# Optimization experiments

Measured on AMD Instinct MI355X. Metric: run time of the kernel, lower is better.

Reference implementation:

```python
import jax, jax.numpy as jnp
import numpy as np
import math

D_MODEL = 512
NUM_HEADS = 8
D_K = D_MODEL // NUM_HEADS
B, S = 4, 2048


def setup_inputs() -> dict:
    key = jax.random.key(0)
    ks = jax.random.split(key, 8)
    scale = 1.0 / math.sqrt(D_MODEL)
    return {
        "q": jax.random.normal(ks[0], (B, S, D_MODEL), jnp.float32),
        "k": jax.random.normal(ks[1], (B, S, D_MODEL), jnp.float32),
        "v": jax.random.normal(ks[2], (B, S, D_MODEL), jnp.float32),
        "mask": jax.random.randint(ks[3], (B, 1, S, S), 0, 2) > 0,
        "w_q": jax.random.normal(ks[4], (D_MODEL, D_MODEL), jnp.float32) * scale,
        "w_k": jax.random.normal(ks[5], (D_MODEL, D_MODEL), jnp.float32) * scale,
        "w_v": jax.random.normal(ks[6], (D_MODEL, D_MODEL), jnp.float32) * scale,
        "w_o": jax.random.normal(ks[7], (D_MODEL, D_MODEL), jnp.float32) * scale,
    }


def reference(q, k, v, mask, w_q, w_k, w_v, w_o):
    # Linear(d_model,d_model,bias=False): y = x @ W^T
    def split_heads(x):  # [B,S,D] -> [B,H,S,Dk]
        return x.reshape(B, S, NUM_HEADS, D_K).transpose(0, 2, 1, 3)

    queries = split_heads(q @ w_q.T)
    keys = split_heads(k @ w_k.T)
    values = split_heads(v @ w_v.T)

    scores = jnp.einsum("bhqd,bhkd->bhqk", queries, keys) / math.sqrt(D_K)
    scores = jnp.where(mask, jnp.float32(-1e9), scores)
    attention_weights = jax.nn.softmax(scores, axis=-1)  # [B,H,S,S]

    attn = jnp.einsum("bhqk,bhkd->bhqd", attention_weights, values)
    attn = attn.transpose(0, 2, 1, 3).reshape(B, S, D_MODEL)
    out = attn @ w_o.T
    return out, attention_weights
```

## Files before the change

### kernel.cpp

```cpp
#include <hip/hip_runtime.h>
#include <hip/hip_bf16.h>
#include <cstdint>

constexpr int B_ = 4;
constexpr int S_ = 2048;
constexpr int D_ = 512;
constexpr int H_ = 8;
constexpr int DK_ = 64;
constexpr int M_ = B_ * S_;

typedef __attribute__((ext_vector_type(8))) short bf16x8;
typedef __attribute__((ext_vector_type(4))) short bf16x4;
typedef __attribute__((ext_vector_type(4))) float f32x4;

__device__ __forceinline__ unsigned short f2bf(float x) {
    unsigned u = __float_as_uint(x);
    return (unsigned short)((u + 0x7fffu + ((u >> 16) & 1u)) >> 16);
}
__device__ __forceinline__ float bf2f(unsigned short h) {
    return __uint_as_float(((unsigned)h) << 16);
}

#define MFMA32(a, b, c) __builtin_amdgcn_mfma_f32_16x16x32_bf16(a, b, c, 0, 0, 0)

__global__ __launch_bounds__(256) void cvt_rm(const float* __restrict__ X,
                                              short* __restrict__ Xh,
                                              short* __restrict__ Xl) {
    size_t idx = ((size_t)blockIdx.x * 256 + threadIdx.x) * 8;
    float4 v0 = *reinterpret_cast<const float4*>(X + idx);
    float4 v1 = *reinterpret_cast<const float4*>(X + idx + 4);
    float f[8] = {v0.x, v0.y, v0.z, v0.w, v1.x, v1.y, v1.z, v1.w};
    short hh[8], ll[8];
#pragma unroll
    for (int e = 0; e < 8; ++e) {
        unsigned short hb = f2bf(f[e]);
        hh[e] = (short)hb;
        ll[e] = (short)f2bf(f[e] - bf2f(hb));
    }
    *(bf16x4*)(Xh + idx)     = (bf16x4){hh[0], hh[1], hh[2], hh[3]};
    *(bf16x4*)(Xh + idx + 4) = (bf16x4){hh[4], hh[5], hh[6], hh[7]};
    *(bf16x4*)(Xl + idx)     = (bf16x4){ll[0], ll[1], ll[2], ll[3]};
    *(bf16x4*)(Xl + idx + 4) = (bf16x4){ll[4], ll[5], ll[6], ll[7]};
}

__device__ __forceinline__ void stage_bf(const short* __restrict__ srcH,
                                         const short* __restrict__ srcL,
                                         short* Hh, short* Hl, int tid, int rows) {
#pragma unroll
    for (int p = 0; p < rows / 32; ++p) {
        int idx = tid + p * 256;
        int r = idx >> 3;
        int cc = idx & 7;
        int off = r * 64 + ((cc ^ (r & 7)) << 3);
        *(bf16x8*)(Hh + off) = *(const bf16x8*)(srcH + (size_t)r * 512 + cc * 8);
        *(bf16x8*)(Hl + off) = *(const bf16x8*)(srcL + (size_t)r * 512 + cc * 8);
    }
}

template <int EPI>
__global__ __launch_bounds__(256) void gemm_bf(const short* __restrict__ Ah_g,
                                               const short* __restrict__ Al_g,
                                               const short* __restrict__ Wh_g,
                                               const short* __restrict__ Wl_g,
                                               float* __restrict__ C,
                                               short* __restrict__ Ch,
                                               short* __restrict__ Cl) {
    __shared__ __align__(16) short Ah[8192];
    __shared__ __align__(16) short Al[8192];
    __shared__ __align__(16) short Wh[4096];
    __shared__ __align__(16) short Wl[4096];

    const int tid = threadIdx.x;
    const int wave = tid >> 6;
    const int lane = tid & 63;
    const int lg = lane >> 4;
    const int lr = lane & 15;
    const int bm = blockIdx.x * 128;
    const int bn = blockIdx.y * 64;

    f32x4 acc[2][4];
#pragma unroll
    for (int s = 0; s < 2; ++s)
#pragma unroll
        for (int n = 0; n < 4; ++n) acc[s][n] = (f32x4){0.f, 0.f, 0.f, 0.f};

    for (int k0 = 0; k0 < 512; k0 += 64) {
        stage_bf(Ah_g + (size_t)bm * 512 + k0, Al_g + (size_t)bm * 512 + k0, Ah, Al, tid, 128);
        stage_bf(Wh_g + (size_t)bn * 512 + k0, Wl_g + (size_t)bn * 512 + k0, Wh, Wl, tid, 64);
        __syncthreads();

#pragma unroll
        for (int ks = 0; ks < 2; ++ks) {
            bf16x8 ah[2], al[2];
#pragma unroll
            for (int sub = 0; sub < 2; ++sub) {
                int r = wave * 32 + sub * 16 + lr;
                int off = r * 64 + (((ks * 4 + lg) ^ (r & 7)) << 3);
                ah[sub] = *(const bf16x8*)(Ah + off);
                al[sub] = *(const bf16x8*)(Al + off);
            }
#pragma unroll
            for (int nsub = 0; nsub < 4; ++nsub) {
                int r = nsub * 16 + lr;
                int off = r * 64 + (((ks * 4 + lg) ^ (r & 7)) << 3);
                bf16x8 wh = *(const bf16x8*)(Wh + off);
                bf16x8 wl = *(const bf16x8*)(Wl + off);
#pragma unroll
                for (int sub = 0; sub < 2; ++sub) {
                    acc[sub][nsub] = MFMA32(ah[sub], wh, acc[sub][nsub]);
                    acc[sub][nsub] = MFMA32(ah[sub], wl, acc[sub][nsub]);
                    acc[sub][nsub] = MFMA32(al[sub], wh, acc[sub][nsub]);
                }
            }
        }
        __syncthreads();
    }

#pragma unroll
    for (int sub = 0; sub < 2; ++sub)
#pragma unroll
        for (int nsub = 0; nsub < 4; ++nsub)
#pragma unroll
            for (int rr = 0; rr < 4; ++rr) {
                int row = bm + wave * 32 + sub * 16 + lg * 4 + rr;
                int col = bn + nsub * 16 + lr;
                float a = acc[sub][nsub][rr];
                if (EPI == 0) {
                    C[(size_t)row * 512 + col] = a;
                } else {
                    unsigned short hb = f2bf(a);
                    size_t off = (((size_t)(row >> 11) * 8 + (col >> 6)) * 2048 +
                                  (row & 2047)) * 64 + (col & 63);
                    Ch[off] = (short)hb;
                    Cl[off] = (short)f2bf(a - bf2f(hb));
                }
            }
}

__global__ __launch_bounds__(256) void vt_kernel(const float* __restrict__ V,
                                                 short* __restrict__ Vt) {
    __shared__ short tile[64][72];
    const int bh = blockIdx.y;
    const int b = bh >> 3, h = bh & 7;
    const int j0 = blockIdx.x * 64;
    const int tid = threadIdx.x;
    {
        int jj = tid >> 2;
        int c = (tid & 3) * 16;
        const float* src = V + ((size_t)(b * 2048 + j0 + jj)) * 512 + h * 64 + c;
#pragma unroll
        for (int q = 0; q < 4; ++q) {
            float4 v = *reinterpret_cast<const float4*>(src + q * 4);
            tile[jj][c + q * 4 + 0] = (short)f2bf(v.x);
            tile[jj][c + q * 4 + 1] = (short)f2bf(v.y);
            tile[jj][c + q * 4 + 2] = (short)f2bf(v.z);
            tile[jj][c + q * 4 + 3] = (short)f2bf(v.w);
        }
    }
    __syncthreads();
    {
        int dk = tid >> 2;
        int jq = (tid & 3) * 16;
        short* dst = Vt + ((size_t)(bh * 64 + dk)) * 2048 + j0 + jq;
#pragma unroll
        for (int q = 0; q < 4; ++q) {
            bf16x4 o = {tile[jq + q * 4 + 0][dk], tile[jq + q * 4 + 1][dk],
                        tile[jq + q * 4 + 2][dk], tile[jq + q * 4 + 3][dk]};
            *(bf16x4*)(dst + q * 4) = o;
        }
    }
}

__global__ __launch_bounds__(256) void mask_pack(const int* __restrict__ mask,
                                                 unsigned long long* __restrict__ pk) {
    const int row = blockIdx.x;
    const int tid = threadIdx.x;
    const int* mrow = mask + (size_t)row * 2048;
#pragma unroll
    for (int p = 0; p < 8; ++p) {
        int j = p * 256 + tid;
        unsigned long long bal = __ballot(mrow[j] != 0);
        if ((tid & 63) == 0) pk[(size_t)row * 32 + p * 4 + (tid >> 6)] = bal;
    }
}

__global__ __launch_bounds__(256, 3) void fused_attn(
    const short* __restrict__ Qh_g, const short* __restrict__ Ql_g,
    const short* __restrict__ Kh_g, const short* __restrict__ Kl_g,
    const short* __restrict__ Vt_g, const unsigned long long* __restrict__ pk,
    float* __restrict__ P, short* __restrict__ Aho, short* __restrict__ Alo) {
    __shared__ __align__(16) short Kbuf[2][2][4096];
    __shared__ __align__(16) short Wt[4096];

    const int tid = threadIdx.x;
    const int wave = tid >> 6;
    const int lane = tid & 63;
    const int lg = lane >> 4;
    const int lr = lane & 15;

    const int wgid = blockIdx.y * 32 + blockIdx.x;
    const int xcd = wgid & 7;
    const int slot = wgid >> 3;
    const int bh = xcd * 4 + (slot & 3);
    const int i0 = (slot >> 2) * 64;
    const int b = bh >> 3;

    bf16x8 qh[2], ql[2];
    {
        const size_t qbase = ((size_t)bh * 2048 + i0 + wave * 16 + lr) * 64;
#pragma unroll
        for (int ks = 0; ks < 2; ++ks) {
            qh[ks] = *(const bf16x8*)(Qh_g + qbase + (ks * 4 + lg) * 8);
            ql[ks] = *(const bf16x8*)(Ql_g + qbase + (ks * 4 + lg) * 8);
        }
    }

    const int o0 = tid * 16;
    const int o1 = 4096 + tid * 16;
    const int s0 = o0 ^ (((o0 >> 7) & 7) << 4);
    const int s1 = o1 ^ (((o1 >> 7) & 7) << 4);

    bf16x8 Rh0, Rh1, Rl0, Rl1;
#define LOADKH(t)                                                           \
    {                                                                       \
        const short* bKh = Kh_g + ((size_t)bh * 2048 + (t) * 64) * 64;      \
        Rh0 = *(const bf16x8*)(bKh + (o0 >> 1));                            \
        Rh1 = *(const bf16x8*)(bKh + (o1 >> 1));                            \
    }
#define WRITEKH(cur)                                                        \
    {                                                                       \
        *(bf16x8*)(&Kbuf[cur][0][0] + (s0 >> 1)) = Rh0;                     \
        *(bf16x8*)(&Kbuf[cur][0][0] + (s1 >> 1)) = Rh1;                     \
    }
#define LOADK(t)                                                            \
    {                                                                       \
        const short* bKh = Kh_g + ((size_t)bh * 2048 + (t) * 64) * 64;      \
        const short* bKl = Kl_g + ((size_t)bh * 2048 + (t) * 64) * 64;      \
        Rh0 = *(const bf16x8*)(bKh + (o0 >> 1));                            \
        Rh1 = *(const bf16x8*)(bKh + (o1 >> 1));                            \
        Rl0 = *(const bf16x8*)(bKl + (o0 >> 1));                            \
        Rl1 = *(const bf16x8*)(bKl + (o1 >> 1));                            \
    }
#define WRITEK(cur)                                                         \
    {                                                                       \
        *(bf16x8*)(&Kbuf[cur][0][0] + (s0 >> 1)) = Rh0;                     \
        *(bf16x8*)(&Kbuf[cur][0][0] + (s1 >> 1)) = Rh1;                     \
        *(bf16x8*)(&Kbuf[cur][1][0] + (s0 >> 1)) = Rl0;                     \
        *(bf16x8*)(&Kbuf[cur][1][0] + (s1 >> 1)) = Rl1;                     \
    }

    const size_t pkrow = (size_t)b * 2048 + i0 + wave * 16 + lg * 4;

    float l_[4] = {0.f, 0.f, 0.f, 0.f};

    LOADKH(0);
    for (int t = 0; t < 32; ++t) {
        const int cur = t & 1;
        WRITEKH(cur);
        if (t < 31) LOADKH(t + 1);
        unsigned long long pkv[4];
#pragma unroll
        for (int rr = 0; rr < 4; ++rr) pkv[rr] = pk[(pkrow + rr) * 32 + t];
        __syncthreads();

        const short* KH = &Kbuf[cur][0][0];
#pragma unroll
        for (int jt = 0; jt < 4; ++jt) {
            f32x4 s = (f32x4){0.f, 0.f, 0.f, 0.f};
            int r = jt * 16 + lr;
#pragma unroll
            for (int ks = 0; ks < 2; ++ks) {
                int off = (r * 128 + (ks * 4 + lg) * 16) ^ ((r & 7) << 4);
                bf16x8 kh = *(const bf16x8*)(KH + (off >> 1));
                s = MFMA32(qh[ks], kh, s);
            }
#pragma unroll
            for (int rr = 0; rr < 4; ++rr) {
                bool mk = (pkv[rr] >> (jt * 16 + lr)) & 1ull;
                l_[rr] += mk ? 0.f : __expf(s[rr] * 0.125f);
            }
        }
    }

#pragma unroll
    for (int rr = 0; rr < 4; ++rr) {
        float l = l_[rr];
#pragma unroll
        for (int d = 1; d < 16; d <<= 1) l += __shfl_xor(l, d);
        l_[rr] = l;
    }

    float invl[4];
#pragma unroll
    for (int rr = 0; rr < 4; ++rr) invl[rr] = 1.0f / fmaxf(l_[rr], 1e-37f);

    f32x4 Oa[4];
#pragma unroll
    for (int dt = 0; dt < 4; ++dt) Oa[dt] = (f32x4){0.f, 0.f, 0.f, 0.f};

    LOADK(0);
    for (int t = 0; t < 32; ++t) {
        const int cur = t & 1;
        WRITEK(cur);
        if (t < 31) LOADK(t + 1);
        unsigned long long pkv[4];
#pragma unroll
        for (int rr = 0; rr < 4; ++rr) pkv[rr] = pk[(pkrow + rr) * 32 + t];
        bf16x8 vf[4][2];
#pragma unroll
        for (int dt = 0; dt < 4; ++dt)
#pragma unroll
            for (int ks2 = 0; ks2 < 2; ++ks2)
                vf[dt][ks2] = *(const bf16x8*)(Vt_g +
                    ((size_t)(bh * 64 + dt * 16 + lr)) * 2048 + t * 64 + (ks2 * 4 + lg) * 8);
        __syncthreads();

        const short* KH = &Kbuf[cur][0][0];
        const short* KL = &Kbuf[cur][1][0];
#pragma unroll
        for (int jt = 0; jt < 4; ++jt) {
            f32x4 s = (f32x4){0.f, 0.f, 0.f, 0.f};
            int r = jt * 16 + lr;
#pragma unroll
            for (int ks = 0; ks < 2; ++ks) {
                int off = (r * 128 + (ks * 4 + lg) * 16) ^ ((r & 7) << 4);
                bf16x8 kh = *(const bf16x8*)(KH + (off >> 1));
                bf16x8 kl = *(const bf16x8*)(KL + (off >> 1));
                s = MFMA32(qh[ks], kh, s);
                s = MFMA32(qh[ks], kl, s);
                s = MFMA32(ql[ks], kh, s);
            }
#pragma unroll
            for (int rr = 0; rr < 4; ++rr) {
                bool mk = (pkv[rr] >> (jt * 16 + lr)) & 1ull;
                float w = mk ? 0.f : __expf(s[rr] * 0.125f) * invl[rr];
                int rw = wave * 16 + lg * 4 + rr;
                int wo = rw * 64 + (((jt * 2 + (lr >> 3)) ^ (rw & 7)) << 3) + (lr & 7);
                Wt[wo] = (short)f2bf(w);
            }
        }

        {
            int rp = wave * 16 + (lane >> 2);
            int c2 = (lane & 3) * 2;
            int po0 = rp * 64 + (((c2 + 0) ^ (rp & 7)) << 3);
            int po1 = rp * 64 + (((c2 + 1) ^ (rp & 7)) << 3);
            bf16x8 wa = *(const bf16x8*)(Wt + po0);
            bf16x8 wb = *(const bf16x8*)(Wt + po1);
            float* Prow = P + ((size_t)bh * 2048 + i0 + rp) * 2048 + t * 64 + (lane & 3) * 16;
#pragma unroll
            for (int q = 0; q < 2; ++q) {
                f32x4 oA = {bf2f((unsigned short)wa[q * 4 + 0]), bf2f((unsigned short)wa[q * 4 + 1]),
                            bf2f((unsigned short)wa[q * 4 + 2]), bf2f((unsigned short)wa[q * 4 + 3])};
                f32x4 oB = {bf2f((unsigned short)wb[q * 4 + 0]), bf2f((unsigned short)wb[q * 4 + 1]),
                            bf2f((unsigned short)wb[q * 4 + 2]), bf2f((unsigned short)wb[q * 4 + 3])};
                *(f32x4*)(Prow + q * 4) = oA;
                *(f32x4*)(Prow + 8 + q * 4) = oB;
            }
        }

        bf16x8 aw[2];
#pragma unroll
        for (int ks2 = 0; ks2 < 2; ++ks2) {
            int ra = wave * 16 + lr;
            int ao = ra * 64 + (((ks2 * 4 + lg) ^ (ra & 7)) << 3);
            aw[ks2] = *(const bf16x8*)(Wt + ao);
        }
#pragma unroll
        for (int dt = 0; dt < 4; ++dt)
#pragma unroll
            for (int ks2 = 0; ks2 < 2; ++ks2)
                Oa[dt] = MFMA32(aw[ks2], vf[dt][ks2], Oa[dt]);
    }

    {
        const int h = bh & 7;
#pragma unroll
        for (int dt = 0; dt < 4; ++dt)
#pragma unroll
            for (int rr = 0; rr < 4; ++rr) {
                int gi = i0 + wave * 16 + lg * 4 + rr;
                size_t off = ((size_t)(b * 2048 + gi)) * 512 + h * 64 + dt * 16 + lr;
                float a = Oa[dt][rr];
                unsigned short hb = f2bf(a);
                Aho[off] = (short)hb;
                Alo[off] = (short)f2bf(a - bf2f(hb));
            }
    }
#undef LOADKH
#undef WRITEKH
#undef LOADK
#undef WRITEK
}

extern "C" void kernel_launch(void* const* d_in, const int* in_sizes, int n_in,
                              void* d_out, int out_size, void* d_ws, size_t ws_size,
                              hipStream_t stream) {
    const float* q   = (const float*)d_in[0];
    const float* k   = (const float*)d_in[1];
    const float* v   = (const float*)d_in[2];
    const int*   msk = (const int*)d_in[3];
    const float* w_q = (const float*)d_in[4];
    const float* w_k = (const float*)d_in[5];
    const float* w_v = (const float*)d_in[6];
    const float* w_o = (const float*)d_in[7];

    float* out = (float*)d_out;
    float* P   = out + (size_t)B_ * S_ * D_;

    short* qh = (short*)d_ws;
    short* ql = qh + (size_t)4194304;
    short* kh = ql + (size_t)4194304;
    short* kl = kh + (size_t)4194304;
    short* vh = kl + (size_t)4194304;
    short* vl = vh + (size_t)4194304;
    short* Qh = vl + (size_t)4194304;
    short* Ql = Qh + (size_t)4194304;
    short* Kh = Ql + (size_t)4194304;
    short* Kl = Kh + (size_t)4194304;
    float* Vf = (float*)(Kl + (size_t)4194304);
    short* Vt = (short*)(Vf + (size_t)M_ * D_);
    unsigned long long* pk = (unsigned long long*)(Vt + (size_t)4194304);
    short* wqh = (short*)(pk + (size_t)262144);
    short* wql = wqh + (size_t)262144;
    short* wkh = wql + (size_t)262144;
    short* wkl = wkh + (size_t)262144;
    short* wvh = wkl + (size_t)262144;
    short* wvl = wvh + (size_t)262144;
    short* woh = wvl + (size_t)262144;
    short* wol = woh + (size_t)262144;

    dim3 blk(256);
    dim3 gproj(M_ / 128, D_ / 64);

    hipLaunchKernelGGL(cvt_rm, dim3(2048), blk, 0, stream, q, qh, ql);
    hipLaunchKernelGGL(cvt_rm, dim3(2048), blk, 0, stream, k, kh, kl);
    hipLaunchKernelGGL(cvt_rm, dim3(2048), blk, 0, stream, v, vh, vl);
    hipLaunchKernelGGL(cvt_rm, dim3(128), blk, 0, stream, w_q, wqh, wql);
    hipLaunchKernelGGL(cvt_rm, dim3(128), blk, 0, stream, w_k, wkh, wkl);
    hipLaunchKernelGGL(cvt_rm, dim3(128), blk, 0, stream, w_v, wvh, wvl);
    hipLaunchKernelGGL(cvt_rm, dim3(128), blk, 0, stream, w_o, woh, wol);

    hipLaunchKernelGGL((gemm_bf<1>), gproj, blk, 0, stream, qh, ql, wqh, wql,
                       (float*)nullptr, Qh, Ql);
    hipLaunchKernelGGL((gemm_bf<1>), gproj, blk, 0, stream, kh, kl, wkh, wkl,
                       (float*)nullptr, Kh, Kl);
    hipLaunchKernelGGL((gemm_bf<0>), gproj, blk, 0, stream, vh, vl, wvh, wvl,
                       Vf, (short*)nullptr, (short*)nullptr);

    hipLaunchKernelGGL(vt_kernel, dim3(32, 32), blk, 0, stream, Vf, Vt);
    hipLaunchKernelGGL(mask_pack, dim3(M_), blk, 0, stream, msk, pk);

    hipLaunchKernelGGL(fused_attn, dim3(32, 32), blk, 0, stream,
                       Qh, Ql, Kh, Kl, Vt, pk, P, qh, ql);

    hipLaunchKernelGGL((gemm_bf<0>), gproj, blk, 0, stream, qh, ql, woh, wol,
                       out, (short*)nullptr, (short*)nullptr);
}
```

Measured before the change: 469.2 us.

## Split fused attention into exp-store pass and normalize-plus-PV pass

Replaces the single fused attention kernel with two kernels. The first computes QK^T scores, masked exponentials and row sums, writing unnormalized bf16 exponentials to a 256 MB workspace buffer E. The second rereads E to write the normalized fp32 probabilities and to compute P·V. This removes the need for a second QK^T pass or online rescaling, but adds a large extra write and read of the intermediate, and it only runs when the workspace is big enough; otherwise the old fused kernel is used.

```diff
diff --git a/kernel.cpp b/kernel.cpp
--- a/kernel.cpp
+++ b/kernel.cpp
@@ -181,6 +181,213 @@
         int j = p * 256 + tid;
         unsigned long long bal = __ballot(mrow[j] != 0);
         if ((tid & 63) == 0) pk[(size_t)row * 32 + p * 4 + (tid >> 6)] = bal;
+    }
+}
+
+__global__ __launch_bounds__(256, 3) void attn_phase1(
+    const short* __restrict__ Qh_g, const short* __restrict__ Ql_g,
+    const short* __restrict__ Kh_g, const short* __restrict__ Kl_g,
+    const unsigned long long* __restrict__ pk,
+    short* __restrict__ E, float* __restrict__ Linv) {
+    __shared__ __align__(16) short Kbuf[2][2][4096];
+    __shared__ __align__(16) short Wt[4096];
+
+    const int tid = threadIdx.x;
+    const int wave = tid >> 6;
+    const int lane = tid & 63;
+    const int lg = lane >> 4;
+    const int lr = lane & 15;
+
+    const int wgid = blockIdx.y * 32 + blockIdx.x;
+    const int xcd = wgid & 7;
+    const int slot = wgid >> 3;
+    const int bh = xcd * 4 + (slot & 3);
+    const int i0 = (slot >> 2) * 64;
+    const int b = bh >> 3;
+
+    bf16x8 qh[2], ql[2];
+    {
+        const size_t qbase = ((size_t)bh * 2048 + i0 + wave * 16 + lr) * 64;
+#pragma unroll
+        for (int ks = 0; ks < 2; ++ks) {
+            qh[ks] = *(const bf16x8*)(Qh_g + qbase + (ks * 4 + lg) * 8);
+            ql[ks] = *(const bf16x8*)(Ql_g + qbase + (ks * 4 + lg) * 8);
+        }
+    }
+
+    const int o0 = tid * 16;
+    const int o1 = 4096 + tid * 16;
+    const int s0 = o0 ^ (((o0 >> 7) & 7) << 4);
+    const int s1 = o1 ^ (((o1 >> 7) & 7) << 4);
+
+    bf16x8 Rh0, Rh1, Rl0, Rl1;
+#define LOADK(t)                                                            \
+    {                                                                       \
+        const short* bKh = Kh_g + ((size_t)bh * 2048 + (t) * 64) * 64;      \
+        const short* bKl = Kl_g + ((size_t)bh * 2048 + (t) * 64) * 64;      \
+        Rh0 = *(const bf16x8*)(bKh + (o0 >> 1));                            \
+        Rh1 = *(const bf16x8*)(bKh + (o1 >> 1));                            \
+        Rl0 = *(const bf16x8*)(bKl + (o0 >> 1));                            \
+        Rl1 = *(const bf16x8*)(bKl + (o1 >> 1));                            \
+    }
+#define WRITEK(cur)                                                         \
+    {                                                                       \
+        *(bf16x8*)(&Kbuf[cur][0][0] + (s0 >> 1)) = Rh0;                     \
+        *(bf16x8*)(&Kbuf[cur][0][0] + (s1 >> 1)) = Rh1;                     \
+        *(bf16x8*)(&Kbuf[cur][1][0] + (s0 >> 1)) = Rl0;                     \
+        *(bf16x8*)(&Kbuf[cur][1][0] + (s1 >> 1)) = Rl1;                     \
+    }
+
+    const size_t pkrow = (size_t)b * 2048 + i0 + wave * 16 + lg * 4;
+    const int rp = wave * 16 + (lane >> 2);
+    const int c2 = (lane & 3) * 2;
+    const int po0 = rp * 64 + (((c2 + 0) ^ (rp & 7)) << 3);
+    const int po1 = rp * 64 + (((c2 + 1) ^ (rp & 7)) << 3);
+
+    float l_[4] = {0.f, 0.f, 0.f, 0.f};
+
+    LOADK(0);
+    for (int t = 0; t < 32; ++t) {
+        const int cur = t & 1;
+        WRITEK(cur);
+        if (t < 31) LOADK(t + 1);
+        unsigned long long pkv[4];
+#pragma unroll
+        for (int rr = 0; rr < 4; ++rr) pkv[rr] = pk[(pkrow + rr) * 32 + t];
+        __syncthreads();
+
+        const short* KH = &Kbuf[cur][0][0];
+        const short* KL = &Kbuf[cur][1][0];
+#pragma unroll
+        for (int jt = 0; jt < 4; ++jt) {
+            f32x4 s = (f32x4){0.f, 0.f, 0.f, 0.f};
+            int r = jt * 16 + lr;
+#pragma unroll
+            for (int ks = 0; ks < 2; ++ks) {
+                int off = (r * 128 + (ks * 4 + lg) * 16) ^ ((r & 7) << 4);
+                bf16x8 kh = *(const bf16x8*)(KH + (off >> 1));
+                bf16x8 kl = *(const bf16x8*)(KL + (off >> 1));
+                s = MFMA32(qh[ks], kh, s);
+                s = MFMA32(qh[ks], kl, s);
+                s = MFMA32(ql[ks], kh, s);
+            }
+#pragma unroll
+            for (int rr = 0; rr < 4; ++rr) {
+                bool mk = (pkv[rr] >> (jt * 16 + lr)) & 1ull;
+                float w = mk ? 0.f : __expf(s[rr] * 0.125f);
+                l_[rr] += w;
+                int rw = wave * 16 + lg * 4 + rr;
+                int wo = rw * 64 + (((jt * 2 + (lr >> 3)) ^ (rw & 7)) << 3) + (lr & 7);
+                Wt[wo] = (short)f2bf(w);
+            }
+        }
+
+        {
+            short* Et = E + ((((size_t)(bh * 32 + (i0 >> 6))) * 32 + t) << 12);
+            bf16x8 wa = *(const bf16x8*)(Wt + po0);
+            bf16x8 wb = *(const bf16x8*)(Wt + po1);
+            *(bf16x8*)(Et + po0) = wa;
+            *(bf16x8*)(Et + po1) = wb;
+        }
+    }
+
+#pragma unroll
+    for (int rr = 0; rr < 4; ++rr) {
+        float l = l_[rr];
+#pragma unroll
+        for (int d = 1; d < 16; d <<= 1) l += __shfl_xor(l, d);
+        if (lr == 0)
+            Linv[(size_t)bh * 2048 + i0 + wave * 16 + lg * 4 + rr] =
+                1.0f / fmaxf(l, 1e-37f);
+    }
+#undef LOADK
+#undef WRITEK
+}
+
+__global__ __launch_bounds__(256) void attn_phase2(
+    const short* __restrict__ E, const float* __restrict__ Linv,
+    const short* __restrict__ Vt_g,
+    float* __restrict__ P, short* __restrict__ Aho, short* __restrict__ Alo) {
+    const int tid = threadIdx.x;
+    const int wave = tid >> 6;
+    const int lane = tid & 63;
+    const int lg = lane >> 4;
+    const int lr = lane & 15;
+
+    const int wgid = blockIdx.y * 32 + blockIdx.x;
+    const int xcd = wgid & 7;
+    const int slot = wgid >> 3;
+    const int bh = xcd * 4 + (slot & 3);
+    const int i0 = (slot >> 2) * 64;
+    const int b = bh >> 3;
+
+    const int rp = wave * 16 + (lane >> 2);
+    const int c2 = (lane & 3) * 2;
+    const int po0 = rp * 64 + (((c2 + 0) ^ (rp & 7)) << 3);
+    const int po1 = rp * 64 + (((c2 + 1) ^ (rp & 7)) << 3);
+    const float invlP = Linv[(size_t)bh * 2048 + i0 + rp];
+
+    const int ra = wave * 16 + lr;
+    const int ao0 = ra * 64 + (((0 * 4 + lg) ^ (ra & 7)) << 3);
+    const int ao1 = ra * 64 + (((1 * 4 + lg) ^ (ra & 7)) << 3);
+
+    float invc[4];
+#pragma unroll
+    for (int rr = 0; rr < 4; ++rr)
+        invc[rr] = Linv[(size_t)bh * 2048 + i0 + wave * 16 + lg * 4 + rr];
+
+    f32x4 Oa[4];
+#pragma unroll
+    for (int dt = 0; dt < 4; ++dt) Oa[dt] = (f32x4){0.f, 0.f, 0.f, 0.f};
+
+    const size_t Ebase = ((size_t)(bh * 32 + (i0 >> 6))) * 32;
+
+    for (int t = 0; t < 32; ++t) {
+        const short* Et = E + ((Ebase + t) << 12);
+
+        bf16x8 wa = *(const bf16x8*)(Et + po0);
+        bf16x8 wb = *(const bf16x8*)(Et + po1);
+        float* Prow = P + ((size_t)bh * 2048 + i0 + rp) * 2048 + t * 64 + (lane & 3) * 16;
+#pragma unroll
+        for (int q = 0; q < 2; ++q) {
+            f32x4 oA = {bf2f((unsigned short)wa[q * 4 + 0]) * invlP,
+                        bf2f((unsigned short)wa[q * 4 + 1]) * invlP,
+                        bf2f((unsigned short)wa[q * 4 + 2]) * invlP,
+                        bf2f((unsigned short)wa[q * 4 + 3]) * invlP};
+            f32x4 oB = {bf2f((unsigned short)wb[q * 4 + 0]) * invlP,
+                        bf2f((unsigned short)wb[q * 4 + 1]) * invlP,
+                        bf2f((unsigned short)wb[q * 4 + 2]) * invlP,
+                        bf2f((unsigned short)wb[q * 4 + 3]) * invlP};
+            *(f32x4*)(Prow + q * 4) = oA;
+            *(f32x4*)(Prow + 8 + q * 4) = oB;
+        }
+
+        bf16x8 aw0 = *(const bf16x8*)(Et + ao0);
+        bf16x8 aw1 = *(const bf16x8*)(Et + ao1);
+#pragma unroll
+        for (int dt = 0; dt < 4; ++dt) {
+            bf16x8 v0 = *(const bf16x8*)(Vt_g +
+                ((size_t)(bh * 64 + dt * 16 + lr)) * 2048 + t * 64 + lg * 8);
+            bf16x8 v1 = *(const bf16x8*)(Vt_g +
+                ((size_t)(bh * 64 + dt * 16 + lr)) * 2048 + t * 64 + 32 + lg * 8);
+            Oa[dt] = MFMA32(aw0, v0, Oa[dt]);
+            Oa[dt] = MFMA32(aw1, v1, Oa[dt]);
+        }
+    }
+
+    {
+        const int h = bh & 7;
+#pragma unroll
+        for (int dt = 0; dt < 4; ++dt)
+#pragma unroll
+            for (int rr = 0; rr < 4; ++rr) {
+                int gi = i0 + wave * 16 + lg * 4 + rr;
+                size_t off = ((size_t)(b * 2048 + gi)) * 512 + h * 64 + dt * 16 + lr;
+                float a = Oa[dt][rr] * invc[rr];
+                unsigned short hb = f2bf(a);
+                Aho[off] = (short)hb;
+                Alo[off] = (short)f2bf(a - bf2f(hb));
+            }
     }
 }
 
@@ -429,6 +636,9 @@
     short* wvl = wvh + (size_t)262144;
     short* woh = wvl + (size_t)262144;
     short* wol = woh + (size_t)262144;
+    float* Linv = (float*)(wol + (size_t)262144);
+    short* E    = (short*)(Linv + (size_t)65536);
+    const size_t NEED = ((char*)(E + (size_t)134217728)) - (char*)d_ws;
 
     dim3 blk(256);
     dim3 gproj(M_ / 128, D_ / 64);
@@ -451,8 +661,15 @@
     hipLaunchKernelGGL(vt_kernel, dim3(32, 32), blk, 0, stream, Vf, Vt);
     hipLaunchKernelGGL(mask_pack, dim3(M_), blk, 0, stream, msk, pk);
 
-    hipLaunchKernelGGL(fused_attn, dim3(32, 32), blk, 0, stream,
-                       Qh, Ql, Kh, Kl, Vt, pk, P, qh, ql);
+    if (ws_size >= NEED) {
+        hipLaunchKernelGGL(attn_phase1, dim3(32, 32), blk, 0, stream,
+                           Qh, Ql, Kh, Kl, pk, E, Linv);
+        hipLaunchKernelGGL(attn_phase2, dim3(32, 32), blk, 0, stream,
+                           E, Linv, Vt, P, qh, ql);
+    } else {
+        hipLaunchKernelGGL(fused_attn, dim3(32, 32), blk, 0, stream,
+                           Qh, Ql, Kh, Kl, Vt, pk, P, qh, ql);
+    }
 
     hipLaunchKernelGGL((gemm_bf<0>), gproj, blk, 0, stream, qh, ql, woh, wol,
                        out, (short*)nullptr, (short*)nullptr);
```

After: 601.6 us. +28.2%, slower.

## Fuse V transpose into V projection epilogue and batch conversion launches

Applied to the files above, without the earlier changes.

The V projection GEMM now writes bf16 transposed Vt directly through a shared-memory staging epilogue, which removes the fp32 Vf intermediate and the separate vt_kernel pass. The seven conversion launches are merged into two kernels indexed by blockIdx.y. This cuts a 16MB fp32 write and read plus several launch overheads. In exchange it reuses the GEMM's A shared buffers with a stride of 66 for the transpose, and the column reads from that buffer may hit LDS bank conflicts.

```diff
diff --git a/kernel.cpp b/kernel.cpp
--- a/kernel.cpp
+++ b/kernel.cpp
@@ -23,10 +23,9 @@
 
 #define MFMA32(a, b, c) __builtin_amdgcn_mfma_f32_16x16x32_bf16(a, b, c, 0, 0, 0)
 
-__global__ __launch_bounds__(256) void cvt_rm(const float* __restrict__ X,
-                                              short* __restrict__ Xh,
-                                              short* __restrict__ Xl) {
-    size_t idx = ((size_t)blockIdx.x * 256 + threadIdx.x) * 8;
+__device__ __forceinline__ void cvt_body(const float* __restrict__ X,
+                                         short* __restrict__ Xh,
+                                         short* __restrict__ Xl, size_t idx) {
     float4 v0 = *reinterpret_cast<const float4*>(X + idx);
     float4 v1 = *reinterpret_cast<const float4*>(X + idx + 4);
     float f[8] = {v0.x, v0.y, v0.z, v0.w, v1.x, v1.y, v1.z, v1.w};
@@ -41,6 +40,34 @@
     *(bf16x4*)(Xh + idx + 4) = (bf16x4){hh[4], hh[5], hh[6], hh[7]};
     *(bf16x4*)(Xl + idx)     = (bf16x4){ll[0], ll[1], ll[2], ll[3]};
     *(bf16x4*)(Xl + idx + 4) = (bf16x4){ll[4], ll[5], ll[6], ll[7]};
+}
+
+__global__ __launch_bounds__(256) void cvt_qkv(
+    const float* __restrict__ q, const float* __restrict__ k,
+    const float* __restrict__ v,
+    short* __restrict__ qh, short* __restrict__ ql,
+    short* __restrict__ kh, short* __restrict__ kl,
+    short* __restrict__ vh, short* __restrict__ vl) {
+    const float* X; short *Xh, *Xl;
+    if (blockIdx.y == 0)      { X = q; Xh = qh; Xl = ql; }
+    else if (blockIdx.y == 1) { X = k; Xh = kh; Xl = kl; }
+    else                      { X = v; Xh = vh; Xl = vl; }
+    cvt_body(X, Xh, Xl, ((size_t)blockIdx.x * 256 + threadIdx.x) * 8);
+}
+
+__global__ __launch_bounds__(256) void cvt_w(
+    const float* __restrict__ wq, const float* __restrict__ wk,
+    const float* __restrict__ wv, const float* __restrict__ wo,
+    short* __restrict__ qh, short* __restrict__ ql,
+    short* __restrict__ kh, short* __restrict__ kl,
+    short* __restrict__ vh, short* __restrict__ vl,
+    short* __restrict__ oh, short* __restrict__ ol) {
+    const float* X; short *Xh, *Xl;
+    if (blockIdx.y == 0)      { X = wq; Xh = qh; Xl = ql; }
+    else if (blockIdx.y == 1) { X = wk; Xh = kh; Xl = kl; }
+    else if (blockIdx.y == 2) { X = wv; Xh = vh; Xl = vl; }
+    else                      { X = wo; Xh = oh; Xl = ol; }
+    cvt_body(X, Xh, Xl, ((size_t)blockIdx.x * 256 + threadIdx.x) * 8);
 }
 
 __device__ __forceinline__ void stage_bf(const short* __restrict__ srcH,
@@ -114,6 +141,38 @@
             }
         }
         __syncthreads();
+    }
+
+    if (EPI == 2) {
+#pragma unroll
+        for (int sub = 0; sub < 2; ++sub)
+#pragma unroll
+            for (int nsub = 0; nsub < 4; ++nsub)
+#pragma unroll
+                for (int rr = 0; rr < 4; ++rr) {
+                    int rloc = wave * 32 + sub * 16 + lg * 4 + rr;
+                    int cloc = nsub * 16 + lr;
+                    short bv = (short)f2bf(acc[sub][nsub][rr]);
+                    if (rloc < 64) Ah[rloc * 66 + cloc] = bv;
+                    else           Al[(rloc - 64) * 66 + cloc] = bv;
+                }
+        __syncthreads();
+        const int dk = tid >> 2;
+        const int j0l = (tid & 3) * 32;
+        const short* src = (j0l < 64) ? Ah : Al;
+        const int jb = j0l & 63;
+        const int h = bn >> 6;
+        const int bq = bm >> 11;
+        short* dst = Ch + ((size_t)((bq * 8 + h) * 64 + dk)) * 2048 + (bm & 2047) + j0l;
+#pragma unroll
+        for (int qq = 0; qq < 4; ++qq) {
+            bf16x8 o;
+#pragma unroll
+            for (int e = 0; e < 8; ++e)
+                o[e] = src[(jb + qq * 8 + e) * 66 + dk];
+            *(bf16x8*)(dst + qq * 8) = o;
+        }
+        return;
     }
 
 #pragma unroll
@@ -137,40 +196,6 @@
             }
 }
 
-__global__ __launch_bounds__(256) void vt_kernel(const float* __restrict__ V,
-                                                 short* __restrict__ Vt) {
-    __shared__ short tile[64][72];
-    const int bh = blockIdx.y;
-    const int b = bh >> 3, h = bh & 7;
-    const int j0 = blockIdx.x * 64;
-    const int tid = threadIdx.x;
-    {
-        int jj = tid >> 2;
-        int c = (tid & 3) * 16;
-        const float* src = V + ((size_t)(b * 2048 + j0 + jj)) * 512 + h * 64 + c;
-#pragma unroll
-        for (int q = 0; q < 4; ++q) {
-            float4 v = *reinterpret_cast<const float4*>(src + q * 4);
-            tile[jj][c + q * 4 + 0] = (short)f2bf(v.x);
-            tile[jj][c + q * 4 + 1] = (short)f2bf(v.y);
-            tile[jj][c + q * 4 + 2] = (short)f2bf(v.z);
-            tile[jj][c + q * 4 + 3] = (short)f2bf(v.w);
-        }
-    }
-    __syncthreads();
-    {
-        int dk = tid >> 2;
-        int jq = (tid & 3) * 16;
-        short* dst = Vt + ((size_t)(bh * 64 + dk)) * 2048 + j0 + jq;
-#pragma unroll
-        for (int q = 0; q < 4; ++q) {
-            bf16x4 o = {tile[jq + q * 4 + 0][dk], tile[jq + q * 4 + 1][dk],
-                        tile[jq + q * 4 + 2][dk], tile[jq + q * 4 + 3][dk]};
-            *(bf16x4*)(dst + q * 4) = o;
-        }
-    }
-}
-
 __global__ __launch_bounds__(256) void mask_pack(const int* __restrict__ mask,
                                                  unsigned long long* __restrict__ pk) {
     const int row = blockIdx.x;
@@ -418,8 +443,7 @@
     short* Ql = Qh + (size_t)4194304;
     short* Kh = Ql + (size_t)4194304;
     short* Kl = Kh + (size_t)4194304;
-    float* Vf = (float*)(Kl + (size_t)4194304);
-    short* Vt = (short*)(Vf + (size_t)M_ * D_);
+    short* Vt = Kl + (size_t)4194304;
     unsigned long long* pk = (unsigned long long*)(Vt + (size_t)4194304);
     short* wqh = (short*)(pk + (size_t)262144);
     short* wql = wqh + (size_t)262144;
@@ -433,22 +457,18 @@
     dim3 blk(256);
     dim3 gproj(M_ / 128, D_ / 64);
 
-    hipLaunchKernelGGL(cvt_rm, dim3(2048), blk, 0, stream, q, qh, ql);
-    hipLaunchKernelGGL(cvt_rm, dim3(2048), blk, 0, stream, k, kh, kl);
-    hipLaunchKernelGGL(cvt_rm, dim3(2048), blk, 0, stream, v, vh, vl);
-    hipLaunchKernelGGL(cvt_rm, dim3(128), blk, 0, stream, w_q, wqh, wql);
-    hipLaunchKernelGGL(cvt_rm, dim3(128), blk, 0, stream, w_k, wkh, wkl);
-    hipLaunchKernelGGL(cvt_rm, dim3(128), blk, 0, stream, w_v, wvh, wvl);
-    hipLaunchKernelGGL(cvt_rm, dim3(128), blk, 0, stream, w_o, woh, wol);
+    hipLaunchKernelGGL(cvt_qkv, dim3(2048, 3), blk, 0, stream,
+                       q, k, v, qh, ql, kh, kl, vh, vl);
+    hipLaunchKernelGGL(cvt_w, dim3(128, 4), blk, 0, stream,
+                       w_q, w_k, w_v, w_o, wqh, wql, wkh, wkl, wvh, wvl, woh, wol);
 
     hipLaunchKernelGGL((gemm_bf<1>), gproj, blk, 0, stream, qh, ql, wqh, wql,
                        (float*)nullptr, Qh, Ql);
     hipLaunchKernelGGL((gemm_bf<1>), gproj, blk, 0, stream, kh, kl, wkh, wkl,
                        (float*)nullptr, Kh, Kl);
-    hipLaunchKernelGGL((gemm_bf<0>), gproj, blk, 0, stream, vh, vl, wvh, wvl,
-                       Vf, (short*)nullptr, (short*)nullptr);
-
-    hipLaunchKernelGGL(vt_kernel, dim3(32, 32), blk, 0, stream, Vf, Vt);
+    hipLaunchKernelGGL((gemm_bf<2>), gproj, blk, 0, stream, vh, vl, wvh, wvl,
+                       (float*)nullptr, Vt, (short*)nullptr);
+
     hipLaunchKernelGGL(mask_pack, dim3(M_), blk, 0, stream, msk, pk);
 
     hipLaunchKernelGGL(fused_attn, dim3(32, 32), blk, 0, stream,
```

After: 452.0 us (median of 2 runs). -3.7%, faster.
